# Optimization experiments

Hardware: AMD Instinct MI355X
Metric: run time of the kernel (lower is better)

Reference implementation:

```python
import jax, jax.numpy as jnp
import numpy as np

GROUP, BS, CH = 16, 8192, 256


def setup_inputs() -> dict:
    key = jax.random.key(0)
    kx, kw = jax.random.split(key)
    x = jax.random.normal(kx, (GROUP, BS, CH), dtype=jnp.float32)
    # PyTorch init: uniform(-stdv, stdv), stdv = 1/sqrt(channels)
    stdv = 1.0 / np.sqrt(CH)
    weight = jax.random.uniform(kw, (GROUP, CH, CH), dtype=jnp.float32,
                                minval=-stdv, maxval=stdv)
    return {"x": x, "weight": weight}


def reference(x, weight):
    # x: (group, bs, n); weight: (group, n, channels). For each column i of
    # weight (w: (group, n)) apply Householder-style reflection sequentially:
    #   x <- x - (2 / (w^T w)) * (x @ w) w^T
    ws = jnp.moveaxis(weight, -1, 0)  # (channels, group, n)

    def step(xc, w):
        denom = jnp.sum(w * w, axis=-1)              # (group,)
        xw = jnp.einsum('gbn,gn->gb', xc, w)         # (group, bs)
        xc = xc - (2.0 / denom)[:, None, None] * xw[..., None] * w[:, None, :]
        return xc, None

    out, _ = jax.lax.scan(step, x, ws)
    return out
```

## Files before the change

### kernel.cpp

```cpp
#include <hip/hip_runtime.h>
#include <hip/hip_bf16.h>

#define GROUPS 16
#define BSZ    8192
#define CHN    256

using f32x4  = __attribute__((ext_vector_type(4))) float;
using bf16x8 = __attribute__((ext_vector_type(8))) __bf16;

static __device__ __forceinline__ unsigned short f32_bf16(float f) {
    unsigned int u = __builtin_bit_cast(unsigned int, f);
    u = (u + 0x7FFFu + ((u >> 16) & 1u)) >> 16;
    return (unsigned short)u;
}
static __device__ __forceinline__ unsigned int pack_bf16x2(float lo, float hi) {
    return (unsigned int)f32_bf16(lo) | ((unsigned int)f32_bf16(hi) << 16);
}

__global__ __launch_bounds__(256) void compose_m(const float* __restrict__ weight,
                                                 unsigned short* __restrict__ Mt) {
    __shared__ float wbuf[16 * 260];
    __shared__ float coefbuf[16];

    const int t    = threadIdx.x;
    const int g    = blockIdx.x >> 4;
    const int r0   = (blockIdx.x & 15) * 16;
    const int lane = t & 15;
    const int rg   = (t >> 4) & 3;
    const int wave = t >> 6;
    const int r    = r0 + wave * 4 + rg;

    float4 m4[4];
#pragma unroll
    for (int j = 0; j < 4; ++j) {
        const int cb = 4 * lane + 64 * j;
        m4[j].x = (cb + 0 == r) ? 1.0f : 0.0f;
        m4[j].y = (cb + 1 == r) ? 1.0f : 0.0f;
        m4[j].z = (cb + 2 == r) ? 1.0f : 0.0f;
        m4[j].w = (cb + 3 == r) ? 1.0f : 0.0f;
    }

    const float* wg = weight + (size_t)g * CHN * CHN;
    const int e16 = t & 15;
    const int nb  = t >> 4;

    for (int iw = 0; iw < 16; ++iw) {
        const int i0 = iw * 16;
        float ld[16];
#pragma unroll
        for (int k = 0; k < 16; ++k)
            ld[k] = wg[(nb + 16 * k) * CHN + i0 + e16];
        __syncthreads();
#pragma unroll
        for (int k = 0; k < 16; ++k)
            wbuf[e16 * 260 + nb + 16 * k] = ld[k];
        __syncthreads();
        {
            const int e = t >> 4;
            float s = 0.0f;
#pragma unroll
            for (int k = 0; k < 16; ++k) {
                const float w = wbuf[e * 260 + lane + 16 * k];
                s += w * w;
            }
            s += __shfl_xor(s, 1);
            s += __shfl_xor(s, 2);
            s += __shfl_xor(s, 4);
            s += __shfl_xor(s, 8);
            if (lane == 0) coefbuf[e] = 2.0f / s;
        }
        __syncthreads();
#pragma unroll
        for (int e = 0; e < 16; ++e) {
            float4 w4[4];
#pragma unroll
            for (int j = 0; j < 4; ++j)
                w4[j] = *(const float4*)&wbuf[e * 260 + 4 * lane + 64 * j];
            float p = 0.0f;
#pragma unroll
            for (int j = 0; j < 4; ++j)
                p += m4[j].x * w4[j].x + m4[j].y * w4[j].y +
                     m4[j].z * w4[j].z + m4[j].w * w4[j].w;
            p += __shfl_xor(p, 1);
            p += __shfl_xor(p, 2);
            p += __shfl_xor(p, 4);
            p += __shfl_xor(p, 8);
            const float s = coefbuf[e] * p;
#pragma unroll
            for (int j = 0; j < 4; ++j) {
                m4[j].x -= s * w4[j].x;
                m4[j].y -= s * w4[j].y;
                m4[j].z -= s * w4[j].z;
                m4[j].w -= s * w4[j].w;
            }
        }
    }

    unsigned short* mg = Mt + (size_t)g * CHN * CHN;
#pragma unroll
    for (int j = 0; j < 4; ++j) {
        const int cb = 4 * lane + 64 * j;
        mg[(size_t)(cb + 0) * CHN + r] = f32_bf16(m4[j].x);
        mg[(size_t)(cb + 1) * CHN + r] = f32_bf16(m4[j].y);
        mg[(size_t)(cb + 2) * CHN + r] = f32_bf16(m4[j].z);
        mg[(size_t)(cb + 3) * CHN + r] = f32_bf16(m4[j].w);
    }
}

__global__ __launch_bounds__(512, 4) void gemm_xm(const float* __restrict__ x,
                                                  const unsigned short* __restrict__ Mt,
                                                  float* __restrict__ out) {
    __shared__ unsigned int xa [128 * 37];
    __shared__ unsigned int mts[256 * 37];

    const int t    = threadIdx.x;
    const int g    = blockIdx.x >> 6;
    const int rb   = blockIdx.x & 63;
    const int r0   = rb * 128;
    const int l    = t & 63;
    const int wave = t >> 6;
    const int wr   = wave >> 2;
    const int wc   = wave & 3;
    const int lm   = l & 15;
    const int q    = l >> 4;

    const float*          xg = x  + ((size_t)g * BSZ + r0) * CHN;
    const unsigned short* mg = Mt +  (size_t)g * CHN * CHN;

    f32x4 acc[4][4];
#pragma unroll
    for (int mi = 0; mi < 4; ++mi)
#pragma unroll
        for (int ni = 0; ni < 4; ++ni)
            acc[mi][ni] = (f32x4){0.f, 0.f, 0.f, 0.f};

    const int srr = t >> 4;
    const int sk4 = t & 15;
    const int mc  = t >> 1;
    const int mh  = t & 1;

    for (int kc = 0; kc < 4; ++kc) {
        const int k0 = kc * 64;
        __syncthreads();
#pragma unroll
        for (int it = 0; it < 4; ++it) {
            const int rr = srr + it * 32;
            const float4 v = *(const float4*)&xg[(size_t)rr * CHN + k0 + 4 * sk4];
            xa[rr * 37 + 2 * sk4 + 0] = pack_bf16x2(v.x, v.y);
            xa[rr * 37 + 2 * sk4 + 1] = pack_bf16x2(v.z, v.w);
        }
        {
            const uint4* src = (const uint4*)(mg + (size_t)mc * CHN + k0 + 32 * mh);
#pragma unroll
            for (int s = 0; s < 4; ++s) {
                const uint4 v = src[s];
                const int base = mc * 37 + 16 * mh + 4 * s;
                mts[base + 0] = v.x;
                mts[base + 1] = v.y;
                mts[base + 2] = v.z;
                mts[base + 3] = v.w;
            }
        }
        __syncthreads();
#pragma unroll
        for (int ks = 0; ks < 2; ++ks) {
            const int koff = 16 * ks + 4 * q;
            bf16x8 a[4], b[4];
#pragma unroll
            for (int mi = 0; mi < 4; ++mi) {
                const int rr = wr * 64 + mi * 16 + lm;
                uint4 u;
                u.x = xa[rr * 37 + koff + 0];
                u.y = xa[rr * 37 + koff + 1];
                u.z = xa[rr * 37 + koff + 2];
                u.w = xa[rr * 37 + koff + 3];
                a[mi] = __builtin_bit_cast(bf16x8, u);
            }
#pragma unroll
            for (int ni = 0; ni < 4; ++ni) {
                const int cc = wc * 64 + ni * 16 + lm;
                uint4 u;
                u.x = mts[cc * 37 + koff + 0];
                u.y = mts[cc * 37 + koff + 1];
                u.z = mts[cc * 37 + koff + 2];
                u.w = mts[cc * 37 + koff + 3];
                b[ni] = __builtin_bit_cast(bf16x8, u);
            }
#pragma unroll
            for (int mi = 0; mi < 4; ++mi)
#pragma unroll
                for (int ni = 0; ni < 4; ++ni)
                    acc[mi][ni] = __builtin_amdgcn_mfma_f32_16x16x32_bf16(
                        a[mi], b[ni], acc[mi][ni], 0, 0, 0);
        }
    }

    float* og = out + ((size_t)g * BSZ + r0) * CHN;
#pragma unroll
    for (int mi = 0; mi < 4; ++mi) {
#pragma unroll
        for (int ni = 0; ni < 4; ++ni) {
            const int col = wc * 64 + ni * 16 + lm;
#pragma unroll
            for (int reg = 0; reg < 4; ++reg) {
                const int row = wr * 64 + mi * 16 + q * 4 + reg;
                og[(size_t)row * CHN + col] = acc[mi][ni][reg];
            }
        }
    }
}

extern "C" void kernel_launch(void* const* d_in, const int* in_sizes, int n_in,
                              void* d_out, int out_size, void* d_ws, size_t ws_size,
                              hipStream_t stream) {
    const float* x = (const float*)d_in[0];
    const float* w = (const float*)d_in[1];
    float* out = (float*)d_out;
    unsigned short* Mt = (unsigned short*)d_ws;

    hipLaunchKernelGGL(compose_m, dim3(GROUPS * 16), dim3(256), 0, stream, w, Mt);
    hipLaunchKernelGGL(gemm_xm,   dim3(GROUPS * 64), dim3(512), 0, stream, x, Mt, out);
}
```

Before: 331.1 us.

## Load GEMM operands straight from global into registers, dropping the LDS staging

The x@M GEMM kernel no longer stages x and Mt tiles through shared memory with barriers. Each wave now loads its own fp32 x fragments and bf16 Mt fragments directly from global memory, converts x to bf16 in registers, and feeds the MFMAs. This removes LDS traffic and block-wide synchronisation. The cost is redundant global/L2 reads, since waves sharing rows or columns each fetch them separately, plus strided per-lane accesses. The launch-bounds occupancy hint drops from 4 to 3.

Result: slower. 372.1 us (+12.4%).

```diff
diff --git a/kernel.cpp b/kernel.cpp
--- a/kernel.cpp
+++ b/kernel.cpp
@@ -107,12 +107,9 @@
     }
 }
 
-__global__ __launch_bounds__(512, 4) void gemm_xm(const float* __restrict__ x,
+__global__ __launch_bounds__(512, 3) void gemm_xm(const float* __restrict__ x,
                                                   const unsigned short* __restrict__ Mt,
                                                   float* __restrict__ out) {
-    __shared__ unsigned int xa [128 * 37];
-    __shared__ unsigned int mts[256 * 37];
-
     const int t    = threadIdx.x;
     const int g    = blockIdx.x >> 6;
     const int rb   = blockIdx.x & 63;
@@ -124,8 +121,8 @@
     const int lm   = l & 15;
     const int q    = l >> 4;
 
-    const float*          xg = x  + ((size_t)g * BSZ + r0) * CHN;
-    const unsigned short* mg = Mt +  (size_t)g * CHN * CHN;
+    const float*          xg = x  + ((size_t)g * BSZ + r0 + wr * 64 + lm) * CHN;
+    const unsigned short* mg = Mt + ((size_t)g * CHN + wc * 64 + lm) * CHN;
 
     f32x4 acc[4][4];
 #pragma unroll
@@ -134,65 +131,42 @@
         for (int ni = 0; ni < 4; ++ni)
             acc[mi][ni] = (f32x4){0.f, 0.f, 0.f, 0.f};
 
-    const int srr = t >> 4;
-    const int sk4 = t & 15;
-    const int mc  = t >> 1;
-    const int mh  = t & 1;
+#pragma unroll 1
+    for (int ks = 0; ks < 8; ++ks) {
+        const int ko = 32 * ks + 8 * q;
 
-    for (int kc = 0; kc < 4; ++kc) {
-        const int k0 = kc * 64;
-        __syncthreads();
+        float4 ax[4][2];
 #pragma unroll
-        for (int it = 0; it < 4; ++it) {
-            const int rr = srr + it * 32;
-            const float4 v = *(const float4*)&xg[(size_t)rr * CHN + k0 + 4 * sk4];
-            xa[rr * 37 + 2 * sk4 + 0] = pack_bf16x2(v.x, v.y);
-            xa[rr * 37 + 2 * sk4 + 1] = pack_bf16x2(v.z, v.w);
+        for (int mi = 0; mi < 4; ++mi) {
+            const float* p = xg + (size_t)(mi * 16) * CHN + ko;
+            ax[mi][0] = *(const float4*)(p);
+            ax[mi][1] = *(const float4*)(p + 4);
         }
-        {
-            const uint4* src = (const uint4*)(mg + (size_t)mc * CHN + k0 + 32 * mh);
+        uint4 bu[4];
 #pragma unroll
-            for (int s = 0; s < 4; ++s) {
-                const uint4 v = src[s];
-                const int base = mc * 37 + 16 * mh + 4 * s;
-                mts[base + 0] = v.x;
-                mts[base + 1] = v.y;
-                mts[base + 2] = v.z;
-                mts[base + 3] = v.w;
-            }
+        for (int ni = 0; ni < 4; ++ni)
+            bu[ni] = *(const uint4*)(mg + (size_t)(ni * 16) * CHN + ko);
+
+        bf16x8 a[4], b[4];
+#pragma unroll
+        for (int mi = 0; mi < 4; ++mi) {
+            uint4 u;
+            u.x = pack_bf16x2(ax[mi][0].x, ax[mi][0].y);
+            u.y = pack_bf16x2(ax[mi][0].z, ax[mi][0].w);
+            u.z = pack_bf16x2(ax[mi][1].x, ax[mi][1].y);
+            u.w = pack_bf16x2(ax[mi][1].z, ax[mi][1].w);
+            a[mi] = __builtin_bit_cast(bf16x8, u);
         }
-        __syncthreads();
 #pragma unroll
-        for (int ks = 0; ks < 2; ++ks) {
-            const int koff = 16 * ks + 4 * q;
-            bf16x8 a[4], b[4];
+        for (int ni = 0; ni < 4; ++ni)
+            b[ni] = __builtin_bit_cast(bf16x8, bu[ni]);
+
 #pragma unroll
-            for (int mi = 0; mi < 4; ++mi) {
-                const int rr = wr * 64 + mi * 16 + lm;
-                uint4 u;
-                u.x = xa[rr * 37 + koff + 0];
-                u.y = xa[rr * 37 + koff + 1];
-                u.z = xa[rr * 37 + koff + 2];
-                u.w = xa[rr * 37 + koff + 3];
-                a[mi] = __builtin_bit_cast(bf16x8, u);
-            }
+        for (int mi = 0; mi < 4; ++mi)
 #pragma unroll
-            for (int ni = 0; ni < 4; ++ni) {
-                const int cc = wc * 64 + ni * 16 + lm;
-                uint4 u;
-                u.x = mts[cc * 37 + koff + 0];
-                u.y = mts[cc * 37 + koff + 1];
-                u.z = mts[cc * 37 + koff + 2];
-                u.w = mts[cc * 37 + koff + 3];
-                b[ni] = __builtin_bit_cast(bf16x8, u);
-            }
-#pragma unroll
-            for (int mi = 0; mi < 4; ++mi)
-#pragma unroll
-                for (int ni = 0; ni < 4; ++ni)
-                    acc[mi][ni] = __builtin_amdgcn_mfma_f32_16x16x32_bf16(
-                        a[mi], b[ni], acc[mi][ni], 0, 0, 0);
-        }
+            for (int ni = 0; ni < 4; ++ni)
+                acc[mi][ni] = __builtin_amdgcn_mfma_f32_16x16x32_bf16(
+                    a[mi], b[ni], acc[mi][ni], 0, 0, 0);
     }
 
     float* og = out + ((size_t)g * BSZ + r0) * CHN;
```
